# Kernel tuning notes

Hardware: AMD Instinct MI355X
Metric: run time of the kernel (lower is better)

Reference implementation:

```python
import jax, jax.numpy as jnp
import numpy as np

N = 50000   # nodes
E = 800000  # edges
F = 128     # input features
H = 4       # heads
C = 32      # hidden per head
ED = 16     # edge_dim
NEG_ATT = 0.2   # GATConv leaky relu slope for attention
NEG_OUT = 0.01  # nn.LeakyReLU default slope in GATLayer


def setup_inputs() -> dict:
    key = jax.random.key(0)
    ks = jax.random.split(key, 9)
    s = 0.05
    return {
        "node_features": jax.random.normal(ks[0], (N, F), jnp.float32),
        "edge_index": jax.random.randint(ks[1], (2, E), 0, N, dtype=jnp.int32),
        "edge_attr": jax.random.normal(ks[2], (E, ED), jnp.float32),
        "W": jax.random.normal(ks[3], (F, H * C), jnp.float32) * s,
        "W_edge": jax.random.normal(ks[4], (ED, H * C), jnp.float32) * s,
        "att_src": jax.random.normal(ks[5], (H, C), jnp.float32) * s,
        "att_dst": jax.random.normal(ks[6], (H, C), jnp.float32) * s,
        "att_edge": jax.random.normal(ks[7], (H, C), jnp.float32) * s,
        "bias": jax.random.normal(ks[8], (H * C,), jnp.float32) * s,
    }


def reference(node_features, edge_index, edge_attr, W, W_edge, att_src, att_dst, att_edge, bias):
    # Project nodes: [N, H, C]  (PyG GATConv with int in_channels shares lin for src/dst)
    x = (node_features @ W).reshape(N, H, C)
    a_src = jnp.einsum('nhc,hc->nh', x, att_src)  # [N, H]
    a_dst = jnp.einsum('nhc,hc->nh', x, att_dst)  # [N, H]

    src, dst = edge_index[0], edge_index[1]

    # add_self_loops with fill_value='mean': self-loop edge_attr = mean of incoming edge attrs
    cnt = jax.ops.segment_sum(jnp.ones((E,), jnp.float32), dst, num_segments=N)
    loop_attr = jax.ops.segment_sum(edge_attr, dst, num_segments=N) / jnp.clip(cnt, 1.0)[:, None]
    ar = jnp.arange(N, dtype=src.dtype)
    src_f = jnp.concatenate([src, ar])          # [E+N]
    dst_f = jnp.concatenate([dst, ar])          # [E+N]
    ea_f = jnp.concatenate([edge_attr, loop_attr], axis=0)  # [E+N, ED]

    # Edge attention contribution
    e = (ea_f @ W_edge).reshape(E + N, H, C)
    a_edge = jnp.einsum('ehc,hc->eh', e, att_edge)  # [E+N, H]

    # Raw attention logits per edge/head, LeakyReLU(0.2)
    alpha = a_src[src_f] + a_dst[dst_f] + a_edge
    alpha = jax.nn.leaky_relu(alpha, NEG_ATT)

    # Softmax over incoming edges per target node (stable; every node has self loop)
    m = jax.ops.segment_max(alpha, dst_f, num_segments=N)      # [N, H]
    ex = jnp.exp(alpha - m[dst_f])                              # [E+N, H]
    denom = jax.ops.segment_sum(ex, dst_f, num_segments=N)     # [N, H]
    attn = ex / denom[dst_f]                                    # [E+N, H]

    # Scatter-aggregate weighted source features
    msgs = x[src_f] * attn[:, :, None]                          # [E+N, H, C]
    out = jax.ops.segment_sum(msgs, dst_f, num_segments=N)      # [N, H, C]
    out = out.reshape(N, H * C) + bias

    # GATLayer wrapper: LeakyReLU(0.01) then Dropout(p=0) (identity)
    return jax.nn.leaky_relu(out, NEG_OUT)
```

## Files before the change

### kernel.cpp

```cpp
#include <hip/hip_runtime.h>

typedef unsigned short u16;
typedef unsigned int u32;
typedef unsigned long long u64;

#define NN 50000
#define EE 800000
#define CAP 48
#define GBLK ((NN+31)/32)

__device__ __forceinline__ float lrelu(float x, float s){ return x>=0.f ? x : s*x; }
__device__ __forceinline__ u16 f2bf(float f){ u32 x=__float_as_uint(f); u32 r=(x+0x7fffu+((x>>16)&1u))>>16; return (u16)r; }
__device__ __forceinline__ float bf2f_lo(u32 u){ union{u32 i; float f;} v; v.i=u<<16; return v.f; }
__device__ __forceinline__ float bf2f_hi(u32 u){ union{u32 i; float f;} v; v.i=u&0xffff0000u; return v.f; }

__global__ __launch_bounds__(256) void k_pre(const float* __restrict__ A,
                                             const float* __restrict__ W,
                                             const float* __restrict__ att_src,
                                             const float* __restrict__ att_dst,
                                             const int*   __restrict__ ei,
                                             const float* __restrict__ ea,
                                             const float* __restrict__ W_edge,
                                             const float* __restrict__ att_edge,
                                             u32* __restrict__ xb,
                                             float* __restrict__ asd,
                                             int* __restrict__ cnt,
                                             u64* __restrict__ csr,
                                             u32* __restrict__ pae){
    __shared__ float Ws[32*128];
    __shared__ float AsT[32*36];
    __shared__ float redS[128];
    __shared__ float redD[128];
    int t = threadIdx.x;
    int bid = blockIdx.x;
    int g = bid / 3, r = bid - g*3;

    if (r == 2){
        int r0 = g * 32;
        int tr = t & 7, tc = t >> 3;
        if (t < 128) redS[t] = 0.f; else redD[t-128] = 0.f;
        float acc[4][4] = {};

        for (int kb = 0; kb < 128; kb += 32){
            {
                int idx = t * 4;
                int rr = idx >> 5, k = idx & 31;
                int row = r0 + rr;
                float4 v = make_float4(0.f,0.f,0.f,0.f);
                if (row < NN) v = *(const float4*)(A + (size_t)row*128 + kb + k);
                AsT[(k+0)*36 + rr] = v.x;
                AsT[(k+1)*36 + rr] = v.y;
                AsT[(k+2)*36 + rr] = v.z;
                AsT[(k+3)*36 + rr] = v.w;
            }
            #pragma unroll
            for (int i = 0; i < 4; i++){
                int idx = (t + i*256) * 4;
                int k = idx >> 7, c = idx & 127;
                *(float4*)&Ws[k*128 + c] = *(const float4*)(W + (size_t)(kb + k)*128 + c);
            }
            __syncthreads();
            #pragma unroll
            for (int k = 0; k < 32; k++){
                float4 av = *(const float4*)&AsT[k*36 + 4*tr];
                float4 wv = *(const float4*)&Ws[k*128 + 4*tc];
                acc[0][0]+=av.x*wv.x; acc[0][1]+=av.x*wv.y; acc[0][2]+=av.x*wv.z; acc[0][3]+=av.x*wv.w;
                acc[1][0]+=av.y*wv.x; acc[1][1]+=av.y*wv.y; acc[1][2]+=av.y*wv.z; acc[1][3]+=av.y*wv.w;
                acc[2][0]+=av.z*wv.x; acc[2][1]+=av.z*wv.y; acc[2][2]+=av.z*wv.z; acc[2][3]+=av.z*wv.w;
                acc[3][0]+=av.w*wv.x; acc[3][1]+=av.w*wv.y; acc[3][2]+=av.w*wv.z; acc[3][3]+=av.w*wv.w;
            }
            __syncthreads();
        }

        int h = tc >> 3;
        float4 as4 = *(const float4*)&att_src[4*tc];
        float4 ad4 = *(const float4*)&att_dst[4*tc];
        #pragma unroll
        for (int i = 0; i < 4; i++){
            float ps = acc[i][0]*as4.x + acc[i][1]*as4.y + acc[i][2]*as4.z + acc[i][3]*as4.w;
            float pd = acc[i][0]*ad4.x + acc[i][1]*ad4.y + acc[i][2]*ad4.z + acc[i][3]*ad4.w;
            atomicAdd(&redS[(4*tr+i)*4 + h], ps);
            atomicAdd(&redD[(4*tr+i)*4 + h], pd);
        }
        #pragma unroll
        for (int i = 0; i < 4; i++){
            int row = r0 + 4*tr + i;
            if (row < NN){
                u32 p0 = (u32)f2bf(acc[i][0]) | ((u32)f2bf(acc[i][1]) << 16);
                u32 p1 = (u32)f2bf(acc[i][2]) | ((u32)f2bf(acc[i][3]) << 16);
                *(uint2*)&xb[(size_t)row*64 + 2*tc] = make_uint2(p0, p1);
            }
        }
        __syncthreads();
        if (t < 128){
            int row = r0 + (t >> 2);
            if (row < NN) asd[row*8 + (t & 3)] = redS[t];
        } else {
            int tt = t - 128;
            int row = r0 + (tt >> 2);
            if (row < NN) asd[row*8 + 4 + (tt & 3)] = redD[tt];
        }
    } else {
        float* wea = redS;
        if (t < 64){
            int hh = t >> 4, d = t & 15;
            float s = 0.f;
            #pragma unroll
            for (int c = 0; c < 32; c++)
                s += W_edge[d*128 + hh*32 + c] * att_edge[hh*32 + c];
            wea[t] = s;
        }
        __syncthreads();

        int e = (g*2 + r)*256 + t;
        if (e >= EE) return;
        int src = ei[e];
        int dst = ei[EE + e];
        const float4* p = (const float4*)(ea + (size_t)e*16);
        float4 q0 = p[0], q1 = p[1], q2 = p[2], q3 = p[3];
        float f[16] = {q0.x,q0.y,q0.z,q0.w, q1.x,q1.y,q1.z,q1.w,
                       q2.x,q2.y,q2.z,q2.w, q3.x,q3.y,q3.z,q3.w};
        float sh[4];
        #pragma unroll
        for (int h = 0; h < 4; h++){
            float s = 0.f;
            #pragma unroll
            for (int d = 0; d < 16; d++) s += f[d]*wea[h*16+d];
            sh[h] = s;
        }
        u32 p01 = (u32)f2bf(sh[0]) | ((u32)f2bf(sh[1]) << 16);
        u32 p23 = (u32)f2bf(sh[2]) | ((u32)f2bf(sh[3]) << 16);
        *(uint2*)&pae[(size_t)e*2] = make_uint2(p01, p23);
        int slot = atomicAdd(&cnt[dst], 1);
        if (slot < CAP)
            __builtin_nontemporal_store(((u64)(u32)src << 32) | (u32)e,
                                        &csr[(size_t)dst*CAP + slot]);
    }
}

__global__ __launch_bounds__(256) void k_agg(const u32* __restrict__ xb,
                                             const float* __restrict__ asd,
                                             const int* __restrict__ cnt,
                                             const u64* __restrict__ csr,
                                             const u32* __restrict__ pae,
                                             const float* __restrict__ bias,
                                             float* __restrict__ out){
    int lane = threadIdx.x & 63, wvi = threadIdx.x >> 6;
    int n = blockIdx.x*4 + wvi;
    if (n >= NN) return;
    int h = lane >> 4, j16 = lane & 15, e4 = lane >> 2, hl = lane & 3;
    int dgc = cnt[n];
    int dg = min(dgc, CAP);
    int start = n*CAP;
    float ad_n = asd[n*8 + 4 + hl];

    float denom = 0.f, acc0 = 0.f, acc1 = 0.f, sum_ae = 0.f;
    for (int base = 0; base < dg; base += 16){
        u64 pr = csr[start + base + j16];
        bool vj = base + j16 < dg;
        int eid = vj ? (int)(pr & 0xffffffffu) : 0;
        int sj  = vj ? (int)(pr >> 32)         : 0;
        int eid_p = __shfl(eid, e4, 64);
        int src_p = __shfl(sj, e4, 64);
        u32 aw = pae[(u32)eid_p*2 + (hl >> 1)];
        float ae = (hl & 1) ? bf2f_hi(aw) : bf2f_lo(aw);
        bool v4 = base + e4 < dg;
        float as_v = asd[src_p*8 + hl];
        float alpha = lrelu(as_v + ad_n + ae, 0.2f);
        float wv = v4 ? __expf(alpha) : 0.f;
        sum_ae += v4 ? ae : 0.f;
        #pragma unroll
        for (int j = 0; j < 16; j++){
            float wj = __shfl(wv, j*4 + h, 64);
            int s   = __shfl(sj, j, 64);
            u32 xp = xb[((u32)s << 6) | lane];
            denom += wj;
            acc0 += wj * bf2f_lo(xp);
            acc1 += wj * bf2f_hi(xp);
        }
    }
    #pragma unroll
    for (int s = 4; s < 64; s <<= 1) sum_ae += __shfl_xor(sum_ae, s, 64);
    float sae = __shfl(sum_ae, h, 64);

    float ael = sae / fmaxf((float)dgc, 1.f);
    float al_loop = lrelu(asd[n*8 + h] + asd[n*8 + 4 + h] + ael, 0.2f);
    float wl = __expf(al_loop);
    u32 xn = xb[((u32)n << 6) | lane];
    denom += wl;
    acc0 += wl * bf2f_lo(xn);
    acc1 += wl * bf2f_hi(xn);

    float inv = 1.f / denom;
    float2 bv = *(const float2*)&bias[2*lane];
    float o0 = lrelu(acc0*inv + bv.x, 0.01f);
    float o1 = lrelu(acc1*inv + bv.y, 0.01f);
    *(float2*)&out[(size_t)n*128 + 2*lane] = make_float2(o0, o1);
}

extern "C" void kernel_launch(void* const* d_in, const int* in_sizes, int n_in,
                              void* d_out, int out_size, void* d_ws, size_t ws_size,
                              hipStream_t stream){
    const float* node_features = (const float*)d_in[0];
    const int*   edge_index    = (const int*)d_in[1];
    const float* edge_attr     = (const float*)d_in[2];
    const float* W             = (const float*)d_in[3];
    const float* W_edge        = (const float*)d_in[4];
    const float* att_src       = (const float*)d_in[5];
    const float* att_dst       = (const float*)d_in[6];
    const float* att_edge      = (const float*)d_in[7];
    const float* bias          = (const float*)d_in[8];
    float* out = (float*)d_out;

    char* p = (char*)d_ws;
    auto alloc = [&](size_t b)->char*{ char* r = p; p += ((b + 255)/256)*256; return r; };
    u32*   xb  = (u32*)  alloc((size_t)NN*64*4);
    float* asd = (float*)alloc((size_t)NN*8*4);
    int*   cnt = (int*)  alloc((size_t)NN*4);
    u64*   csr = (u64*)  alloc((size_t)NN*CAP*8);
    u32*   pae = (u32*)  alloc((size_t)EE*8);

    (void)hipMemsetAsync(cnt, 0, (size_t)NN*4, stream);

    k_pre<<<dim3(3*GBLK), dim3(256), 0, stream>>>(
        node_features, W, att_src, att_dst,
        edge_index, edge_attr, W_edge, att_edge,
        xb, asd, cnt, csr, pae);
    k_agg<<<dim3((NN+3)/4), dim3(256), 0, stream>>>(
        xb, asd, cnt, csr, pae, bias, out);
}
```

Measured before the change: 232.3 us.

## Use bf16 MFMA for node projection GEMM in k_pre

Replaces the scalar FP32 register-tiled GEMM for node_features@W with bf16 MFMA 16x16x32 instructions. Inputs and weights are converted to bf16 and stored in MFMA-fragment layout in shared memory, with W double-buffered across K blocks. The attention dot products and bf16 output stores are reorganised to match the MFMA accumulator layout. This lowers FP32 ALU cost in the projection but adds bf16 rounding of inputs and weights, plus scattered 16-bit global stores.

```diff
diff --git a/kernel.cpp b/kernel.cpp
--- a/kernel.cpp
+++ b/kernel.cpp
@@ -3,6 +3,8 @@
 typedef unsigned short u16;
 typedef unsigned int u32;
 typedef unsigned long long u64;
+typedef short bf16x8 __attribute__((ext_vector_type(8)));
+typedef float f32x4  __attribute__((ext_vector_type(4)));
 
 #define NN 50000
 #define EE 800000
@@ -27,8 +29,8 @@
                                              int* __restrict__ cnt,
                                              u64* __restrict__ csr,
                                              u32* __restrict__ pae){
-    __shared__ float Ws[32*128];
-    __shared__ float AsT[32*36];
+    __shared__ u16 AF[4096];
+    __shared__ u16 WK[2][4096];
     __shared__ float redS[128];
     __shared__ float redD[128];
     int t = threadIdx.x;
@@ -37,58 +39,77 @@
 
     if (r == 2){
         int r0 = g * 32;
-        int tr = t & 7, tc = t >> 3;
+        int w = t >> 6, l = t & 63;
         if (t < 128) redS[t] = 0.f; else redD[t-128] = 0.f;
-        float acc[4][4] = {};
-
-        for (int kb = 0; kb < 128; kb += 32){
-            {
-                int idx = t * 4;
-                int rr = idx >> 5, k = idx & 31;
-                int row = r0 + rr;
-                float4 v = make_float4(0.f,0.f,0.f,0.f);
-                if (row < NN) v = *(const float4*)(A + (size_t)row*128 + kb + k);
-                AsT[(k+0)*36 + rr] = v.x;
-                AsT[(k+1)*36 + rr] = v.y;
-                AsT[(k+2)*36 + rr] = v.z;
-                AsT[(k+3)*36 + rr] = v.w;
+
+        #pragma unroll
+        for (int it = 0; it < 4; it++){
+            int idx = (t + it*256) * 4;
+            int rr = idx >> 7, k = idx & 127;
+            int row = r0 + rr;
+            float4 v = make_float4(0.f,0.f,0.f,0.f);
+            if (row < NN) v = *(const float4*)(A + (size_t)row*128 + k);
+            int rh = rr >> 4, kk = k >> 5;
+            int lanef = (rr & 15) + (((k >> 3) & 3) << 4);
+            int j4 = k & 7;
+            u32 p0 = (u32)f2bf(v.x) | ((u32)f2bf(v.y) << 16);
+            u32 p1 = (u32)f2bf(v.z) | ((u32)f2bf(v.w) << 16);
+            *(uint2*)&AF[(((rh*4 + kk)*64 + lanef) << 3) + j4] = make_uint2(p0, p1);
+        }
+
+        auto stageW = [&](int kb, int b){
+            #pragma unroll
+            for (int it = 0; it < 4; it++){
+                int idx = (t + it*256) * 4;
+                int kr = idx >> 7, c = idx & 127;
+                float4 v = *(const float4*)(W + (size_t)(kb*32 + kr)*128 + c);
+                int ct = c >> 4;
+                int lanef = (c & 15) + (((kr >> 3) & 3) << 4);
+                int j = kr & 7;
+                u16* base = &WK[b][((ct*64 + lanef) << 3) + j];
+                base[0]  = f2bf(v.x);
+                base[8]  = f2bf(v.y);
+                base[16] = f2bf(v.z);
+                base[24] = f2bf(v.w);
             }
-            #pragma unroll
-            for (int i = 0; i < 4; i++){
-                int idx = (t + i*256) * 4;
-                int k = idx >> 7, c = idx & 127;
-                *(float4*)&Ws[k*128 + c] = *(const float4*)(W + (size_t)(kb + k)*128 + c);
+        };
+
+        stageW(0, 0);
+        __syncthreads();
+
+        int rh = w >> 1, ctb = (w & 1) * 4;
+        f32x4 acc[4] = {};
+        for (int kb = 0; kb < 4; kb++){
+            if (kb < 3) stageW(kb+1, (kb+1)&1);
+            bf16x8 af = *(bf16x8*)&AF[((rh*4 + kb)*64 + l) << 3];
+            #pragma unroll
+            for (int c4 = 0; c4 < 4; c4++){
+                bf16x8 bfr = *(bf16x8*)&WK[kb&1][((ctb + c4)*64 + l) << 3];
+                acc[c4] = __builtin_amdgcn_mfma_f32_16x16x32_bf16(af, bfr, acc[c4], 0, 0, 0);
             }
             __syncthreads();
-            #pragma unroll
-            for (int k = 0; k < 32; k++){
-                float4 av = *(const float4*)&AsT[k*36 + 4*tr];
-                float4 wv = *(const float4*)&Ws[k*128 + 4*tc];
-                acc[0][0]+=av.x*wv.x; acc[0][1]+=av.x*wv.y; acc[0][2]+=av.x*wv.z; acc[0][3]+=av.x*wv.w;
-                acc[1][0]+=av.y*wv.x; acc[1][1]+=av.y*wv.y; acc[1][2]+=av.y*wv.z; acc[1][3]+=av.y*wv.w;
-                acc[2][0]+=av.z*wv.x; acc[2][1]+=av.z*wv.y; acc[2][2]+=av.z*wv.z; acc[2][3]+=av.z*wv.w;
-                acc[3][0]+=av.w*wv.x; acc[3][1]+=av.w*wv.y; acc[3][2]+=av.w*wv.z; acc[3][3]+=av.w*wv.w;
-            }
-            __syncthreads();
-        }
-
-        int h = tc >> 3;
-        float4 as4 = *(const float4*)&att_src[4*tc];
-        float4 ad4 = *(const float4*)&att_dst[4*tc];
-        #pragma unroll
-        for (int i = 0; i < 4; i++){
-            float ps = acc[i][0]*as4.x + acc[i][1]*as4.y + acc[i][2]*as4.z + acc[i][3]*as4.w;
-            float pd = acc[i][0]*ad4.x + acc[i][1]*ad4.y + acc[i][2]*ad4.z + acc[i][3]*ad4.w;
-            atomicAdd(&redS[(4*tr+i)*4 + h], ps);
-            atomicAdd(&redD[(4*tr+i)*4 + h], pd);
-        }
-        #pragma unroll
-        for (int i = 0; i < 4; i++){
-            int row = r0 + 4*tr + i;
-            if (row < NN){
-                u32 p0 = (u32)f2bf(acc[i][0]) | ((u32)f2bf(acc[i][1]) << 16);
-                u32 p1 = (u32)f2bf(acc[i][2]) | ((u32)f2bf(acc[i][3]) << 16);
-                *(uint2*)&xb[(size_t)row*64 + 2*tc] = make_uint2(p0, p1);
+        }
+
+        int h0 = ctb >> 1;
+        float as0 = att_src[(ctb+0)*16 + (l&15)], ad0 = att_dst[(ctb+0)*16 + (l&15)];
+        float as1 = att_src[(ctb+1)*16 + (l&15)], ad1 = att_dst[(ctb+1)*16 + (l&15)];
+        float as2 = att_src[(ctb+2)*16 + (l&15)], ad2 = att_dst[(ctb+2)*16 + (l&15)];
+        float as3 = att_src[(ctb+3)*16 + (l&15)], ad3 = att_dst[(ctb+3)*16 + (l&15)];
+        #pragma unroll
+        for (int reg = 0; reg < 4; reg++){
+            int lr = rh*16 + (l >> 4)*4 + reg;
+            int gr = r0 + lr;
+            float x0 = acc[0][reg], x1 = acc[1][reg], x2 = acc[2][reg], x3 = acc[3][reg];
+            atomicAdd(&redS[lr*4 + h0],     x0*as0 + x1*as1);
+            atomicAdd(&redS[lr*4 + h0 + 1], x2*as2 + x3*as3);
+            atomicAdd(&redD[lr*4 + h0],     x0*ad0 + x1*ad1);
+            atomicAdd(&redD[lr*4 + h0 + 1], x2*ad2 + x3*ad3);
+            if (gr < NN){
+                u16* xo = (u16*)xb + (size_t)gr*128 + (l & 15);
+                xo[(ctb+0)*16] = f2bf(x0);
+                xo[(ctb+1)*16] = f2bf(x1);
+                xo[(ctb+2)*16] = f2bf(x2);
+                xo[(ctb+3)*16] = f2bf(x3);
             }
         }
         __syncthreads();
```

Measured after the change: 267.0 us. 14.9% more time.
